# Kernel tuning notes

Hardware: AMD Instinct MI355X
Metric: run time of the kernel (lower is better)

## Reference

```python
import jax, jax.numpy as jnp
import numpy as np

N, E, D_IN, HID, OUT, H = 20000, 320000, 128, 128, 128, 4

def _lin(key, fan_in, fan_out):
    kw, kb = jax.random.split(key)
    W = jax.random.normal(kw, (fan_in, fan_out), jnp.float32) * 0.05
    b = jax.random.normal(kb, (fan_out,), jnp.float32) * 0.05
    return W, b

def setup_inputs() -> dict:
    key = jax.random.key(0)
    ks = jax.random.split(key, 10)
    x = jax.random.normal(ks[0], (N, D_IN), jnp.float32)
    edge_index = jax.random.randint(ks[1], (2, E), 0, N, jnp.int32)
    # Layer 0: TransformerConv(D_IN -> HID, heads=H, concat=True)
    Wq0, bq0 = _lin(ks[2], D_IN, H * HID)
    Wk0, bk0 = _lin(ks[3], D_IN, H * HID)
    Wv0, bv0 = _lin(ks[4], D_IN, H * HID)
    Ws0, bs0 = _lin(ks[5], D_IN, H * HID)   # root/skip projection
    # Layer 1: TransformerConv(H*HID -> OUT, heads=H, concat=False)
    Wq1, bq1 = _lin(ks[6], H * HID, H * OUT)
    Wk1, bk1 = _lin(ks[7], H * HID, H * OUT)
    Wv1, bv1 = _lin(ks[8], H * HID, H * OUT)
    Ws1, bs1 = _lin(ks[9], H * HID, OUT)    # skip maps to OUT when concat=False
    return dict(x=x, edge_index=edge_index,
                Wq0=Wq0, bq0=bq0, Wk0=Wk0, bk0=bk0, Wv0=Wv0, bv0=bv0, Ws0=Ws0, bs0=bs0,
                Wq1=Wq1, bq1=bq1, Wk1=Wk1, bk1=bk1, Wv1=Wv1, bv1=bv1, Ws1=Ws1, bs1=bs1)

def _transformer_conv(x, src, dst, Wq, bq, Wk, bk, Wv, bv, Ws, bs, heads, out_ch, concat):
    n = x.shape[0]
    q = (x @ Wq + bq).reshape(n, heads, out_ch)
    k = (x @ Wk + bk).reshape(n, heads, out_ch)
    v = (x @ Wv + bv).reshape(n, heads, out_ch)
    # per-edge attention logits: [E, H]
    alpha = jnp.einsum('ehc,ehc->eh', q[dst], k[src]) / jnp.sqrt(jnp.float32(out_ch))
    # softmax grouped by destination node (numerically stable)
    m = jax.ops.segment_max(alpha, dst, num_segments=n)        # [N, H]
    alpha = jnp.exp(alpha - m[dst])
    s = jax.ops.segment_sum(alpha, dst, num_segments=n)       # [N, H]
    alpha = alpha / (s[dst] + 1e-16)
    # weighted scatter-add of messages: [N, H, C]
    out = jax.ops.segment_sum(alpha[..., None] * v[src], dst, num_segments=n)
    if concat:
        out = out.reshape(n, heads * out_ch)
    else:
        out = out.mean(axis=1)
    return out + x @ Ws + bs  # root weight (skip connection)

def reference(x, edge_index,
              Wq0, bq0, Wk0, bk0, Wv0, bv0, Ws0, bs0,
              Wq1, bq1, Wk1, bk1, Wv1, bv1, Ws1, bs1):
    src, dst = edge_index[0], edge_index[1]
    h = _transformer_conv(x, src, dst, Wq0, bq0, Wk0, bk0, Wv0, bv0, Ws0, bs0, H, HID, True)
    h = jax.nn.relu(h)  # dropout is identity in eval mode
    out = _transformer_conv(h, src, dst, Wq1, bq1, Wk1, bk1, Wv1, bv1, Ws1, bs1, H, OUT, False)
    return out
```

## Files before the change

### kernel.cpp

```cpp
#include <hip/hip_runtime.h>
#include <hip/hip_bf16.h>
#include <math.h>

#define HCH    512
#define OUTD   128
#define N0CAT  2048
#define N1CAT  1664
#define P0STR  1024
#define P1STR  640
#define KVW    1024
#define DCAP   64

typedef __attribute__((ext_vector_type(8))) short short8v;
typedef __attribute__((ext_vector_type(8))) unsigned short ushort8v;
typedef __attribute__((ext_vector_type(4))) unsigned short ushort4v;
typedef __attribute__((ext_vector_type(4))) float floatx4;
typedef __attribute__((ext_vector_type(2))) float floatx2;
typedef __attribute__((ext_vector_type(4))) unsigned int uintx4;

__device__ inline float bf2f(unsigned short u) {
    return __uint_as_float(((unsigned)u) << 16);
}

__device__ inline unsigned short f2bf(float f) {
    return (unsigned short)__bfloat16_as_ushort(__float2bfloat16(f));
}

template <bool HI>
__device__ inline floatx2 fp8x2_to_f32(unsigned int w) {
    return __builtin_amdgcn_cvt_pk_f32_fp8(w, HI);
}

__device__ inline unsigned int f32x4_to_fp8(float a, float b, float c, float d) {
    int w = __builtin_amdgcn_cvt_pk_fp8_f32(a, b, 0, false);
    w = __builtin_amdgcn_cvt_pk_fp8_f32(c, d, w, true);
    return (unsigned int)w;
}

__device__ inline void gload_lds16(const void* g, void* l) {
    __builtin_amdgcn_global_load_lds(
        (const __attribute__((address_space(1))) unsigned int*)g,
        (__attribute__((address_space(3))) unsigned int*)l, 16, 0, 0);
}


__device__ void tpose_tile(const float* __restrict__ W, __hip_bfloat16* __restrict__ o,
                           int K, int C, int bx, int by, int t, float (*tile)[33],
                           int pmode) {
    int c0 = bx * 32, k0 = by * 32;
    int tx = t & 31, ty = t >> 5;
    #pragma unroll
    for (int r = ty; r < 32; r += 8)
        tile[r][tx] = W[(size_t)(k0 + r) * C + c0 + tx];
    __syncthreads();
    #pragma unroll
    for (int r = ty; r < 32; r += 8) {
        int col = c0 + r;
        if (pmode) col = ((col >> 3) << 4) + (col & 7) + ((pmode == 2) ? 8 : 0);
        o[(size_t)col * K + k0 + tx] = __float2bfloat16(tile[tx][r]);
    }
}

__global__ __launch_bounds__(256) void prep_all(
        const float* __restrict__ x, __hip_bfloat16* __restrict__ Xb,
        const float* __restrict__ Wq0, const float* __restrict__ Wk0,
        const float* __restrict__ Wv0, const float* __restrict__ Ws0,
        const float* __restrict__ Wq1, const float* __restrict__ Wk1,
        const float* __restrict__ Wv1, const float* __restrict__ Ws1,
        const float* __restrict__ bq0, const float* __restrict__ bk0,
        const float* __restrict__ bv0, const float* __restrict__ bs0,
        const float* __restrict__ bq1, const float* __restrict__ bk1,
        const float* __restrict__ bv1, const float* __restrict__ bs1,
        __hip_bfloat16* __restrict__ Wc0, __hip_bfloat16* __restrict__ Wc1,
        float* __restrict__ bc0, float* __restrict__ bc1,
        int* __restrict__ deg, int* __restrict__ srcs,
        const int* __restrict__ srce, const int* __restrict__ dste,
        int N, int E) {
    __shared__ float tile[32][33];
    int t = threadIdx.x;
    int b = blockIdx.x;
    int nb_cast = (N * 128 + 255) >> 8;
    if (b < nb_cast) {
        int i = b * 256 + t;
        if (i < N * 128) Xb[i] = __float2bfloat16(x[i]);
        return;
    }
    b -= nb_cast;
    if (b < 256) {
        int z = b >> 6, rem = b & 63;
        const float* W = (z == 0) ? Wq0 : (z == 1) ? Wk0 : (z == 2) ? Wv0 : Ws0;
        int base = (z == 0) ? 0 : (z == 3) ? 1536 : 512;
        int pmode = (z == 1) ? 1 : (z == 2) ? 2 : 0;
        tpose_tile(W, Wc0 + (size_t)base * 128, 128, 512, rem & 15, rem >> 4, t, tile, pmode);
        return;
    }
    b -= 256;
    if (b < 768) {
        int z = b >> 8, rem = b & 255;
        const float* W = (z == 0) ? Wq1 : (z == 1) ? Wk1 : Wv1;
        int base = (z == 0) ? 0 : 512;
        int pmode = (z == 1) ? 1 : (z == 2) ? 2 : 0;
        tpose_tile(W, Wc1 + (size_t)base * 512, 512, 512, rem & 15, rem >> 4, t, tile, pmode);
        return;
    }
    b -= 768;
    if (b < 64) {
        tpose_tile(Ws1, Wc1 + (size_t)1536 * 512, 512, 128, b & 3, b >> 2, t, tile, 0);
        return;
    }
    b -= 64;
    if (b < 8) {
        int i = b * 256 + t;
        if (i < N0CAT) {
            int sel = i >> 9, col = i & 511;
            const float* bb = (sel == 0) ? bq0 : (sel == 1) ? bk0 : (sel == 2) ? bv0 : bs0;
            int d = (sel == 0) ? i
                  : (sel == 3) ? i
                  : 512 + ((col >> 3) << 4) + (col & 7) + ((sel == 2) ? 8 : 0);
            bc0[d] = bb[col];
        }
        if (i < N1CAT) {
            if (i < 1536) {
                int sel = i >> 9, col = i & 511;
                const float* bb = (sel == 0) ? bq1 : (sel == 1) ? bk1 : bv1;
                int d = (sel == 0) ? i
                      : 512 + ((col >> 3) << 4) + (col & 7) + ((sel == 2) ? 8 : 0);
                bc1[d] = bb[col];
            } else {
                bc1[i] = bs1[i - 1536];
            }
        }
        return;
    }
    b -= 8;
    {
        int e = b * 256 + t;
        if (e < E) {
            int d = dste[e];
            int pos = atomicAdd(&deg[d], 1);
            if (pos < DCAP) srcs[d * DCAP + pos] = srce[e];
        }
    }
}


#define BM 128
#define BN 128
#define BK 64

__global__ __launch_bounds__(256) void gemm_mfma(const __hip_bfloat16* __restrict__ A,
                                                 const __hip_bfloat16* __restrict__ Bt,
                                                 const float* __restrict__ bias,
                                                 __hip_bfloat16* __restrict__ P,
                                                 int pstride,
                                                 unsigned char* __restrict__ KV8,
                                                 int M, int K, int Nd, int mt_pad) {
    __shared__ __hip_bfloat16 As[BM][BK];
    __shared__ __hip_bfloat16 Bs[BN][BK];
    int f = blockIdx.x;
    int mt = f % mt_pad, nt = f / mt_pad;
    int bm = mt * BM, bn = nt * BN;
    if (bm >= M) return;
    int t = threadIdx.x;
    int lane = t & 63, w = t >> 6;
    int quad = lane >> 4, l16 = lane & 15;
    int wm = (w >> 1) * 64, wn = (w & 1) * 64;

    int srow = w * 8 + (lane >> 3);
    int c8g = (lane & 7) ^ ((lane >> 3) & 7);
    const char* Ab = (const char*)(A + (size_t)(bm + srow) * K + c8g * 8);
    const char* Bb = (const char*)(Bt + (size_t)(bn + srow) * K + c8g * 8);
    char* Al = (char*)&As[0][0] + w * 1024;
    char* Bl = (char*)&Bs[0][0] + w * 1024;

    int sw = l16 & 7;

    floatx4 acc[4][4];
    #pragma unroll
    for (int i = 0; i < 4; i++)
        #pragma unroll
        for (int j = 0; j < 4; j++)
            acc[i][j] = (floatx4)0.0f;

    for (int k0 = 0; k0 < K; k0 += BK) {
        __syncthreads();
        #pragma unroll
        for (int i = 0; i < 4; i++) {
            size_t go = ((size_t)i * 32 * K + k0) * 2;
            gload_lds16(Ab + go, Al + i * 4096);
            gload_lds16(Bb + go, Bl + i * 4096);
        }
        __syncthreads();
        #pragma unroll
        for (int ks = 0; ks < BK; ks += 32) {
            int c8a = (quad + (ks >> 3)) ^ sw;
            short8v af[4], bfr[4];
            #pragma unroll
            for (int i = 0; i < 4; i++)
                af[i] = *(const short8v*)&As[wm + i * 16 + l16][c8a * 8];
            #pragma unroll
            for (int j = 0; j < 4; j++)
                bfr[j] = *(const short8v*)&Bs[wn + j * 16 + l16][c8a * 8];
            #pragma unroll
            for (int i = 0; i < 4; i++)
                #pragma unroll
                for (int j = 0; j < 4; j++)
                    acc[i][j] = __builtin_amdgcn_mfma_f32_16x16x32_bf16(bfr[j], af[i], acc[i][j], 0, 0, 0);
        }
    }

    #pragma unroll
    for (int i = 0; i < 4; i++) {
        int row = bm + wm + i * 16 + l16;
        if (row >= M) continue;
        #pragma unroll
        for (int j = 0; j < 4; j++) {
            int col = bn + wn + j * 16 + quad * 4;
            floatx4 bv = *(const floatx4*)(bias + col);
            float v0 = acc[i][j][0] + bv[0];
            float v1 = acc[i][j][1] + bv[1];
            float v2 = acc[i][j][2] + bv[2];
            float v3 = acc[i][j][3] + bv[3];
            if (col < 512) {
                ushort4v o = { f2bf(v0), f2bf(v1), f2bf(v2), f2bf(v3) };
                *(ushort4v*)(P + (size_t)row * pstride + col) = o;
            } else if (col < 1536) {
                *(unsigned int*)(KV8 + (size_t)row * KVW + (col - 512)) = f32x4_to_fp8(v0, v1, v2, v3);
            } else {
                ushort4v o = { f2bf(v0), f2bf(v1), f2bf(v2), f2bf(v3) };
                *(ushort4v*)(P + (size_t)row * pstride + 512 + (col - 1536)) = o;
            }
        }
    }
}


#define PF 4

__global__ __launch_bounds__(256) void attn_kernel(const __hip_bfloat16* __restrict__ P,
                                                   int pstride,
                                                   const unsigned char* __restrict__ KV8,
                                                   const int* __restrict__ deg,
                                                   const int* __restrict__ srcs,
                                                   __hip_bfloat16* __restrict__ out_b,
                                                   float* __restrict__ out_f,
                                                   int n_nodes, int mode) {
    int wave = threadIdx.x >> 6;
    int lane = threadIdx.x & 63;
    int node = blockIdx.x * 4 + wave;
    if (node >= n_nodes) return;
    const float qsc = 0.08838834764831845f * 1.4426950408889634f;

    const __hip_bfloat16* Prow = P + (size_t)node * pstride;
    floatx2 q2[4];
    {
        ushort8v qu = *(const ushort8v*)(Prow + lane * 8);
        #pragma unroll
        for (int j = 0; j < 4; j++) {
            q2[j][0] = bf2f(qu[2 * j])     * qsc;
            q2[j][1] = bf2f(qu[2 * j + 1]) * qsc;
        }
    }

    float l = 0.f;
    floatx2 acc2[4];
    #pragma unroll
    for (int j = 0; j < 4; j++) acc2[j] = (floatx2)0.0f;

    int cnt = deg[node];
    if (cnt > DCAP) cnt = DCAP;
    const int* ep = srcs + (size_t)node * DCAP;
    const unsigned char* Kb = KV8 + lane * 16;

    uintx4 kv[PF];
    #pragma unroll
    for (int i = 0; i < PF; i++) {
        if (i < cnt) {
            int s = ep[i];
            kv[i] = *(const uintx4*)(Kb + (size_t)s * KVW);
        }
    }

    int e = 0;
    for (; e + PF <= cnt; e += PF) {
        #pragma unroll
        for (int i = 0; i < PF; i++) {
            uintx4 u = kv[i];
            int pe = e + i + PF;
            if (pe < cnt) {
                int s = ep[pe];
                kv[i] = *(const uintx4*)(Kb + (size_t)s * KVW);
            }
            floatx2 k01 = fp8x2_to_f32<false>(u[0]);
            floatx2 k23 = fp8x2_to_f32<true >(u[0]);
            floatx2 k45 = fp8x2_to_f32<false>(u[1]);
            floatx2 k67 = fp8x2_to_f32<true >(u[1]);
            floatx2 d2 = q2[0] * k01;
            d2 += q2[1] * k23;
            d2 += q2[2] * k45;
            d2 += q2[3] * k67;
            float part = d2[0] + d2[1];
            part += __shfl_xor(part, 1);
            part += __shfl_xor(part, 2);
            part += __shfl_xor(part, 4);
            part += __shfl_xor(part, 8);
            float p = exp2f(part);
            l += p;
            floatx2 pv = { p, p };
            floatx2 v01 = fp8x2_to_f32<false>(u[2]);
            floatx2 v23 = fp8x2_to_f32<true >(u[2]);
            floatx2 v45 = fp8x2_to_f32<false>(u[3]);
            floatx2 v67 = fp8x2_to_f32<true >(u[3]);
            acc2[0] += pv * v01;
            acc2[1] += pv * v23;
            acc2[2] += pv * v45;
            acc2[3] += pv * v67;
        }
    }
    #pragma unroll
    for (int i = 0; i < PF; i++) {
        if (e + i < cnt) {
            uintx4 u = kv[i];
            floatx2 k01 = fp8x2_to_f32<false>(u[0]);
            floatx2 k23 = fp8x2_to_f32<true >(u[0]);
            floatx2 k45 = fp8x2_to_f32<false>(u[1]);
            floatx2 k67 = fp8x2_to_f32<true >(u[1]);
            floatx2 d2 = q2[0] * k01;
            d2 += q2[1] * k23;
            d2 += q2[2] * k45;
            d2 += q2[3] * k67;
            float part = d2[0] + d2[1];
            part += __shfl_xor(part, 1);
            part += __shfl_xor(part, 2);
            part += __shfl_xor(part, 4);
            part += __shfl_xor(part, 8);
            float p = exp2f(part);
            l += p;
            floatx2 pv = { p, p };
            floatx2 v01 = fp8x2_to_f32<false>(u[2]);
            floatx2 v23 = fp8x2_to_f32<true >(u[2]);
            floatx2 v45 = fp8x2_to_f32<false>(u[3]);
            floatx2 v67 = fp8x2_to_f32<true >(u[3]);
            acc2[0] += pv * v01;
            acc2[1] += pv * v23;
            acc2[2] += pv * v45;
            acc2[3] += pv * v67;
        }
    }
    float inv = (l > 0.f) ? 1.f / l : 0.f;

    if (mode == 0) {
        ushort8v su = *(const ushort8v*)(Prow + 512 + lane * 8);
        ushort8v o;
        #pragma unroll
        for (int j = 0; j < 8; j++) {
            float r = fmaxf(acc2[j >> 1][j & 1] * inv + bf2f(su[j]), 0.f);
            o[j] = f2bf(r);
        }
        *(ushort8v*)(out_b + (size_t)node * HCH + lane * 8) = o;
    } else {
        float r[8];
        #pragma unroll
        for (int j = 0; j < 8; j++) {
            r[j] = acc2[j >> 1][j & 1] * inv;
            r[j] += __shfl_xor(r[j], 16);
            r[j] += __shfl_xor(r[j], 32);
            r[j] *= 0.25f;
        }
        if (lane < 16) {
            const __hip_bfloat16* sp = Prow + 512 + lane * 8;
            float* op = out_f + (size_t)node * OUTD + lane * 8;
            #pragma unroll
            for (int j = 0; j < 8; j++) op[j] = r[j] + bf2f(__bfloat16_as_ushort(sp[j]));
        }
    }
}


static inline size_t align256(size_t x) { return (x + 255) & ~(size_t)255; }

extern "C" void kernel_launch(void* const* d_in, const int* in_sizes, int n_in,
                              void* d_out, int out_size, void* d_ws, size_t ws_size,
                              hipStream_t stream) {
    const float* x   = (const float*)d_in[0];
    const int*   ei  = (const int*)d_in[1];
    const float* Wq0 = (const float*)d_in[2];  const float* bq0 = (const float*)d_in[3];
    const float* Wk0 = (const float*)d_in[4];  const float* bk0 = (const float*)d_in[5];
    const float* Wv0 = (const float*)d_in[6];  const float* bv0 = (const float*)d_in[7];
    const float* Ws0 = (const float*)d_in[8];  const float* bs0 = (const float*)d_in[9];
    const float* Wq1 = (const float*)d_in[10]; const float* bq1 = (const float*)d_in[11];
    const float* Wk1 = (const float*)d_in[12]; const float* bk1 = (const float*)d_in[13];
    const float* Wv1 = (const float*)d_in[14]; const float* bv1 = (const float*)d_in[15];
    const float* Ws1 = (const float*)d_in[16]; const float* bs1 = (const float*)d_in[17];
    float* out = (float*)d_out;

    const int N = in_sizes[0] / 128;
    const int E = in_sizes[1] / 2;
    const int* src = ei;
    const int* dst = ei + E;

    int mtiles = (N + BM - 1) / BM;
    int mt_pad = (mtiles + 7) & ~7;
    const int Mpad = mt_pad * BM;

    char* ws = (char*)d_ws;
    __hip_bfloat16* P0  = (__hip_bfloat16*)ws; ws += align256((size_t)N * P0STR * 2);
    __hip_bfloat16* P1  = P0;
    __hip_bfloat16* Hbb = (__hip_bfloat16*)ws; ws += align256((size_t)Mpad * HCH * 2);
    __hip_bfloat16* Xb  = (__hip_bfloat16*)ws; ws += align256((size_t)Mpad * 128 * 2);
    unsigned char* KV8  = (unsigned char*)ws;  ws += align256((size_t)N * KVW);
    __hip_bfloat16* Wc0 = (__hip_bfloat16*)ws; ws += align256((size_t)N0CAT * 128 * 2);
    __hip_bfloat16* Wc1 = (__hip_bfloat16*)ws; ws += align256((size_t)N1CAT * 512 * 2);
    float* bc0 = (float*)ws; ws += align256((size_t)N0CAT * 4);
    float* bc1 = (float*)ws; ws += align256((size_t)N1CAT * 4);
    int* deg    = (int*)ws; ws += align256((size_t)N * 4);
    int* srcs   = (int*)ws; ws += align256((size_t)N * DCAP * 4);

    dim3 blk(256);

    hipMemsetAsync(deg, 0, (size_t)N * 4, stream);

    int nb_cast = (N * 128 + 255) / 256;
    int nb_bucket = (E + 255) / 256;
    int nb_prep = nb_cast + 256 + 768 + 64 + 8 + nb_bucket;
    prep_all<<<nb_prep, blk, 0, stream>>>(
        x, Xb, Wq0, Wk0, Wv0, Ws0, Wq1, Wk1, Wv1, Ws1,
        bq0, bk0, bv0, bs0, bq1, bk1, bv1, bs1,
        Wc0, Wc1, bc0, bc1, deg, srcs, src, dst, N, E);

    gemm_mfma<<<dim3(mt_pad * (N0CAT / BN)), blk, 0, stream>>>(
        Xb, Wc0, bc0, P0, P0STR, KV8, N, 128, N0CAT, mt_pad);
    attn_kernel<<<(N + 3) / 4, blk, 0, stream>>>(P0, P0STR, KV8, deg, srcs, Hbb, nullptr, N, 0);

    gemm_mfma<<<dim3(mt_pad * (N1CAT / BN)), blk, 0, stream>>>(
        Hbb, Wc1, bc1, P1, P1STR, KV8, N, 512, N1CAT, mt_pad);
    attn_kernel<<<(N + 3) / 4, blk, 0, stream>>>(P1, P1STR, KV8, deg, srcs, nullptr, out, N, 1);
}
```

Baseline: 317.0 us.

## Add triple-buffered 256x128 MFMA GEMM with direct-to-LDS loads for layer one

Adds a new 512-thread GEMM kernel for the K=512 layer-1 projection. It uses 256x128 tiles and a three-stage LDS ring fed by direct global-to-LDS loads. Prefetches are interleaved with MFMA phases under explicit barriers and priority hints, aiming to hide memory latency and raise MFMA utilisation. The epilogue is factored into a shared store helper. Larger tiles and one block per CU mean fewer blocks and a risk of tail imbalance.

```diff
diff --git a/kernel.cpp b/kernel.cpp
--- a/kernel.cpp
+++ b/kernel.cpp
@@ -144,6 +144,27 @@
 }
 
 
+__device__ inline void gemm_store(floatx4 a, const float* __restrict__ bias,
+                                  __hip_bfloat16* __restrict__ P, int pstride,
+                                  unsigned char* __restrict__ KV8,
+                                  int row, int col) {
+    floatx4 bv = *(const floatx4*)(bias + col);
+    float v0 = a[0] + bv[0];
+    float v1 = a[1] + bv[1];
+    float v2 = a[2] + bv[2];
+    float v3 = a[3] + bv[3];
+    if (col < 512) {
+        ushort4v o = { f2bf(v0), f2bf(v1), f2bf(v2), f2bf(v3) };
+        *(ushort4v*)(P + (size_t)row * pstride + col) = o;
+    } else if (col < 1536) {
+        *(unsigned int*)(KV8 + (size_t)row * KVW + (col - 512)) = f32x4_to_fp8(v0, v1, v2, v3);
+    } else {
+        ushort4v o = { f2bf(v0), f2bf(v1), f2bf(v2), f2bf(v3) };
+        *(ushort4v*)(P + (size_t)row * pstride + 512 + (col - 1536)) = o;
+    }
+}
+
+
 #define BM 128
 #define BN 128
 #define BK 64
@@ -214,23 +235,128 @@
         int row = bm + wm + i * 16 + l16;
         if (row >= M) continue;
         #pragma unroll
-        for (int j = 0; j < 4; j++) {
-            int col = bn + wn + j * 16 + quad * 4;
-            floatx4 bv = *(const floatx4*)(bias + col);
-            float v0 = acc[i][j][0] + bv[0];
-            float v1 = acc[i][j][1] + bv[1];
-            float v2 = acc[i][j][2] + bv[2];
-            float v3 = acc[i][j][3] + bv[3];
-            if (col < 512) {
-                ushort4v o = { f2bf(v0), f2bf(v1), f2bf(v2), f2bf(v3) };
-                *(ushort4v*)(P + (size_t)row * pstride + col) = o;
-            } else if (col < 1536) {
-                *(unsigned int*)(KV8 + (size_t)row * KVW + (col - 512)) = f32x4_to_fp8(v0, v1, v2, v3);
-            } else {
-                ushort4v o = { f2bf(v0), f2bf(v1), f2bf(v2), f2bf(v3) };
-                *(ushort4v*)(P + (size_t)row * pstride + 512 + (col - 1536)) = o;
+        for (int j = 0; j < 4; j++)
+            gemm_store(acc[i][j], bias, P, pstride, KV8, row, bn + wn + j * 16 + quad * 4);
+    }
+}
+
+
+#define BM8 256
+#define BN8 128
+#define NK8 8
+#define K8  512
+#define ABUF 32768
+#define BBUF 16384
+#define BUFSZ 49152
+
+__global__ __launch_bounds__(512, 1) void gemm_mfma_8ph(
+        const __hip_bfloat16* __restrict__ A,
+        const __hip_bfloat16* __restrict__ Bt,
+        const float* __restrict__ bias,
+        __hip_bfloat16* __restrict__ P, int pstride,
+        unsigned char* __restrict__ KV8,
+        int M, int mt_pad) {
+    __shared__ __align__(16) char smem[3 * BUFSZ];
+    int f = blockIdx.x;
+    int mt = f % mt_pad, nt = f / mt_pad;
+    int bm = mt * BM8, bn = nt * BN8;
+    if (bm >= M) return;
+    int t = threadIdx.x;
+    int lane = t & 63, w = t >> 6;
+    int quad = lane >> 4, l16 = lane & 15;
+    int wm = (w >> 1) * 64, wn = (w & 1) * 64;
+    int sw = l16 & 7;
+
+    int srow = w * 8 + (lane >> 3);
+    int c8g = (lane & 7) ^ ((lane >> 3) & 7);
+    const char* Ab = (const char*)(A + (size_t)(bm + srow) * K8 + c8g * 8);
+    const char* Bb = (const char*)(Bt + (size_t)(bn + srow) * K8 + c8g * 8);
+    char* Al = smem + w * 1024;
+    char* Bl = smem + ABUF + w * 1024;
+
+    floatx4 acc[4][4];
+    #pragma unroll
+    for (int i = 0; i < 4; i++)
+        #pragma unroll
+        for (int j = 0; j < 4; j++)
+            acc[i][j] = (floatx4)0.0f;
+
+    #pragma unroll
+    for (int i = 0; i < 4; i++) gload_lds16(Ab + (size_t)i * 65536, Al + i * 8192);
+    #pragma unroll
+    for (int i = 0; i < 2; i++) gload_lds16(Bb + (size_t)i * 65536, Bl + i * 8192);
+    #pragma unroll
+    for (int i = 0; i < 4; i++) gload_lds16(Ab + (size_t)i * 65536 + 128, Al + BUFSZ + i * 8192);
+    #pragma unroll
+    for (int i = 0; i < 2; i++) gload_lds16(Bb + (size_t)i * 65536 + 128, Bl + BUFSZ + i * 8192);
+    asm volatile("s_waitcnt vmcnt(6)" ::: "memory");
+    __builtin_amdgcn_sched_barrier(0);
+    __builtin_amdgcn_s_barrier();
+    __builtin_amdgcn_sched_barrier(0);
+
+    #pragma unroll
+    for (int tt = 0; tt < NK8; tt++) {
+        const int rd = tt % 3;
+        const int st = (tt + 2) % 3;
+        const bool pre = (tt + 2 < NK8);
+        const __hip_bfloat16* Ar = (const __hip_bfloat16*)(smem + rd * BUFSZ);
+        const __hip_bfloat16* Br = (const __hip_bfloat16*)(smem + rd * BUFSZ + ABUF);
+        #pragma unroll
+        for (int ph = 0; ph < 2; ph++) {
+            int c8a = (quad + ph * 4) ^ sw;
+            short8v af[4], bfr[4];
+            #pragma unroll
+            for (int i = 0; i < 4; i++)
+                af[i] = *(const short8v*)(Ar + (size_t)(wm + i * 16 + l16) * 64 + c8a * 8);
+            #pragma unroll
+            for (int j = 0; j < 4; j++)
+                bfr[j] = *(const short8v*)(Br + (size_t)(wn + j * 16 + l16) * 64 + c8a * 8);
+            if (pre) {
+                size_t ko = (size_t)(tt + 2) * 128;
+                char* Ast = Al + st * BUFSZ;
+                char* Bst = Bl + st * BUFSZ;
+                if (ph == 0) {
+                    gload_lds16(Ab + ko, Ast);
+                    gload_lds16(Ab + 65536 + ko, Ast + 8192);
+                    gload_lds16(Bb + ko, Bst);
+                } else {
+                    gload_lds16(Ab + 131072 + ko, Ast + 16384);
+                    gload_lds16(Ab + 196608 + ko, Ast + 24576);
+                    gload_lds16(Bb + 65536 + ko, Bst + 8192);
+                }
             }
-        }
+            __builtin_amdgcn_sched_barrier(0);
+            __builtin_amdgcn_s_barrier();
+            __builtin_amdgcn_sched_barrier(0);
+            __builtin_amdgcn_s_setprio(1);
+            #pragma unroll
+            for (int i = 0; i < 4; i++)
+                #pragma unroll
+                for (int j = 0; j < 4; j++)
+                    acc[i][j] = __builtin_amdgcn_mfma_f32_16x16x32_bf16(bfr[j], af[i], acc[i][j], 0, 0, 0);
+            __builtin_amdgcn_s_setprio(0);
+            __builtin_amdgcn_sched_barrier(0);
+            if (ph == 0) {
+                __builtin_amdgcn_s_barrier();
+                __builtin_amdgcn_sched_barrier(0);
+            }
+        }
+        if (tt < NK8 - 1) {
+            if (pre) { asm volatile("s_waitcnt vmcnt(6)" ::: "memory"); }
+            else     { asm volatile("s_waitcnt vmcnt(0)" ::: "memory"); }
+            __builtin_amdgcn_sched_barrier(0);
+            __builtin_amdgcn_s_barrier();
+            __builtin_amdgcn_sched_barrier(0);
+        }
+    }
+
+    #pragma unroll
+    for (int i = 0; i < 4; i++) {
+        int row = bm + wm + i * 16 + l16;
+        if (row >= M) continue;
+        #pragma unroll
+        for (int j = 0; j < 4; j++)
+            gemm_store(acc[i][j], bias, P, pstride, KV8, row, bn + wn + j * 16 + quad * 4);
     }
 }
 
@@ -402,6 +528,7 @@
     int mtiles = (N + BM - 1) / BM;
     int mt_pad = (mtiles + 7) & ~7;
     const int Mpad = mt_pad * BM;
+    int mt_pad8 = ((N + BM8 - 1) / BM8 + 7) & ~7;
 
     char* ws = (char*)d_ws;
     __hip_bfloat16* P0  = (__hip_bfloat16*)ws; ws += align256((size_t)N * P0STR * 2);
@@ -432,7 +559,7 @@
         Xb, Wc0, bc0, P0, P0STR, KV8, N, 128, N0CAT, mt_pad);
     attn_kernel<<<(N + 3) / 4, blk, 0, stream>>>(P0, P0STR, KV8, deg, srcs, Hbb, nullptr, N, 0);
 
-    gemm_mfma<<<dim3(mt_pad * (N1CAT / BN)), blk, 0, stream>>>(
-        Hbb, Wc1, bc1, P1, P1STR, KV8, N, 512, N1CAT, mt_pad);
+    gemm_mfma_8ph<<<dim3(mt_pad8 * (N1CAT / BN8)), dim3(512), 0, stream>>>(
+        Hbb, Wc1, bc1, P1, P1STR, KV8, N, mt_pad8);
     attn_kernel<<<(N + 3) / 4, blk, 0, stream>>>(P1, P1STR, KV8, deg, srcs, nullptr, out, N, 1);
 }
```

After: 326.0 us. +2.9%, slower.
